# Kernel optimization log

Hardware: AMD Instinct MI355X
Metric: run time of the kernel (lower is better)

## Reference

```python
import jax, jax.numpy as jnp
import numpy as np

HIDDEN = 100


def gcn_conv(x, W, b, src, dst, w, n):
    # GCNConv with symmetric normalization (self-loops already appended).
    xw = x @ W                                   # [N, H]
    deg = jax.ops.segment_sum(w, dst, num_segments=n)
    dinv = jnp.where(deg > 0, jax.lax.rsqrt(deg), 0.0)
    norm = dinv[src] * w * dinv[dst]             # [E]
    agg = jax.ops.segment_sum(norm[:, None] * xw[src], dst, num_segments=n)
    return agg + b


def setup_inputs() -> dict:
    key = jax.random.key(0)
    ks = jax.random.split(key, 16)
    N, F, E, H = 100000, 128, 1600000, HIDDEN
    x = jax.random.normal(ks[0], (N, F), dtype=jnp.float32)
    edge_index = jax.random.randint(ks[1], (2, E), 0, N, dtype=jnp.int64)
    edge_weight = jax.random.uniform(ks[2], (E,), dtype=jnp.float32)
    sF = 1.0 / np.sqrt(F)
    sH2 = 1.0 / np.sqrt(2 * H)
    sH = 1.0 / np.sqrt(H)
    inp = {
        "x": x, "edge_index": edge_index, "edge_weight": edge_weight,
        "Wcz": jax.random.normal(ks[3], (F, H), jnp.float32) * sF,
        "bcz": jnp.zeros((H,), jnp.float32),
        "Wcr": jax.random.normal(ks[4], (F, H), jnp.float32) * sF,
        "bcr": jnp.zeros((H,), jnp.float32),
        "Wch": jax.random.normal(ks[5], (F, H), jnp.float32) * sF,
        "bch": jnp.zeros((H,), jnp.float32),
        "Wlz": jax.random.normal(ks[6], (2 * H, H), jnp.float32) * sH2,
        "blz": jnp.zeros((H,), jnp.float32),
        "Wlr": jax.random.normal(ks[7], (2 * H, H), jnp.float32) * sH2,
        "blr": jnp.zeros((H,), jnp.float32),
        "Wlh": jax.random.normal(ks[8], (2 * H, H), jnp.float32) * sH2,
        "blh": jnp.zeros((H,), jnp.float32),
        "Wout": jax.random.normal(ks[9], (H, 1), jnp.float32) * sH,
        "bout": jnp.zeros((1,), jnp.float32),
    }
    return inp


def reference(x, edge_index, edge_weight,
              Wcz, bcz, Wcr, bcr, Wch, bch,
              Wlz, blz, Wlr, blr, Wlh, blh,
              Wout, bout):
    N = x.shape[0]
    # add self-loops with weight 1 (GCNConv default)
    loop = jnp.arange(N, dtype=edge_index.dtype)
    src = jnp.concatenate([edge_index[0], loop])
    dst = jnp.concatenate([edge_index[1], loop])
    w = jnp.concatenate([edge_weight, jnp.ones((N,), edge_weight.dtype)])

    H0 = jnp.zeros((N, HIDDEN), x.dtype)  # TGCN initial hidden state

    cz = gcn_conv(x, Wcz, bcz, src, dst, w, N)
    Z = jax.nn.sigmoid(jnp.concatenate([cz, H0], axis=1) @ Wlz + blz)

    cr = gcn_conv(x, Wcr, bcr, src, dst, w, N)
    R = jax.nn.sigmoid(jnp.concatenate([cr, H0], axis=1) @ Wlr + blr)

    ch = gcn_conv(x, Wch, bch, src, dst, w, N)
    Ht = jnp.tanh(jnp.concatenate([ch, H0 * R], axis=1) @ Wlh + blh)

    Hn = Z * H0 + (1.0 - Z) * Ht
    h = jax.nn.relu(Hn)
    return h @ Wout + bout
```

## Files before the change

### kernel.cpp

```cpp
#include <hip/hip_runtime.h>

#define FEAT 128
#define HID  100
#define CHUNK 4096

typedef __attribute__((ext_vector_type(8))) short short8;
typedef __attribute__((ext_vector_type(4))) float f32x4;

__device__ __forceinline__ unsigned short f2bf(float f) {
    union { float f; unsigned int u; } v; v.f = f;
    unsigned int r = v.u + 0x7fffu + ((v.u >> 16) & 1u);
    return (unsigned short)(r >> 16);
}

__device__ __forceinline__ int get_edge(const void* ei, int f64, long long pos) {
    return f64 ? (int)((const long long*)ei)[pos] : ((const int*)ei)[pos];
}

__device__ __forceinline__ int detect_f64(const void* ei) {
    const int* p = (const int*)ei;
    unsigned long long b = __ballot(p[2 * (threadIdx.x & 63) + 1] == 0);
    return b == ~0ull;
}

__global__ __launch_bounds__(256)
void k_cvtfold(const float* __restrict__ x, uint4* __restrict__ xb, int n8,
               const float* __restrict__ Wcz, const float* __restrict__ bcz,
               const float* __restrict__ Wch, const float* __restrict__ bch,
               const float* __restrict__ Wlz, const float* __restrict__ blz,
               const float* __restrict__ Wlh, const float* __restrict__ blh,
               const float* __restrict__ Wout,
               unsigned short* __restrict__ WB, float* __restrict__ bfold_ext,
               float* __restrict__ WoutZ) {
    const int CVTB = 1024;
    if (blockIdx.x < CVTB) {
        int stride = CVTB * 256;
        for (int i = blockIdx.x * 256 + threadIdx.x; i < n8; i += stride) {
            float4 a = *(const float4*)(x + (size_t)i * 8);
            float4 b = *(const float4*)(x + (size_t)i * 8 + 4);
            uint4 o;
            o.x = f2bf(a.x) | ((unsigned)f2bf(a.y) << 16);
            o.y = f2bf(a.z) | ((unsigned)f2bf(a.w) << 16);
            o.z = f2bf(b.x) | ((unsigned)f2bf(b.y) << 16);
            o.w = f2bf(b.z) | ((unsigned)f2bf(b.w) << 16);
            xb[i] = o;
        }
        return;
    }
    int idx = (blockIdx.x - CVTB) * 256 + threadIdx.x;
    if (idx < FEAT * 256) {
        int k = idx >> 8, n = idx & 255;
        float val = 0.f;
        if (n < HID) {
            for (int m = 0; m < HID; m++) val += Wcz[k * HID + m] * Wlz[m * HID + n];
        } else if (n >= 128 && n < 128 + HID) {
            int c = n - 128;
            for (int m = 0; m < HID; m++) val += Wch[k * HID + m] * Wlh[m * HID + c];
        }
        int ni = n >> 4, lc = n & 15, ks = k >> 5, hi = (k >> 3) & 3, j = k & 7;
        WB[(((ni * 4 + ks) * 64 + hi * 16 + lc) << 3) + j] = f2bf(val);
    } else if (idx < FEAT * 256 + 256) {
        int c = idx - FEAT * 256;
        float v = 0.f;
        if (c < HID) {
            v = blz[c];
            for (int j = 0; j < HID; j++) v += bcz[j] * Wlz[j * HID + c];
        } else if (c >= 128 && c < 128 + HID) {
            int cc = c - 128;
            v = blh[cc];
            for (int j = 0; j < HID; j++) v += bch[j] * Wlh[j * HID + cc];
        }
        bfold_ext[c] = v;
    } else if (idx < FEAT * 256 + 256 + 128) {
        int c = idx - FEAT * 256 - 256;
        WoutZ[c] = (c < HID) ? Wout[c] : 0.f;
    }
}

__global__ __launch_bounds__(256)
void k_hist(const void* ei, int* __restrict__ bucketCnt, int* __restrict__ blockBase,
            int NB, int E) {
    int f64 = detect_f64(ei);
    __shared__ int hist[1024];
    int t = threadIdx.x;
    for (int i = t; i < NB; i += 256) hist[i] = 0;
    __syncthreads();
    int e0 = blockIdx.x * CHUNK;
#pragma unroll
    for (int k = 0; k < CHUNK / 256; k++) {
        int e = e0 + k * 256 + t;
        if (e < E) {
            int d = get_edge(ei, f64, (long long)E + e);
            atomicAdd(&hist[d >> 8], 1);
        }
    }
    __syncthreads();
    int* bb = blockBase + (size_t)blockIdx.x * NB;
    for (int b = t; b < NB; b += 256) {
        int c = hist[b];
        if (c) bb[b] = atomicAdd(&bucketCnt[b], c);
    }
}

__global__ void k_scanb(const int* __restrict__ bucketCnt, int* __restrict__ bucketStart,
                        int NB) {
    __shared__ int lds[1024];
    int t = threadIdx.x;
    int v = (t < NB) ? bucketCnt[t] : 0;
    lds[t] = v;
    __syncthreads();
    for (int off = 1; off < 1024; off <<= 1) {
        int tv = (t >= off) ? lds[t - off] : 0;
        __syncthreads();
        lds[t] += tv;
        __syncthreads();
    }
    if (t < NB) bucketStart[t] = lds[t] - v;
    if (t == NB - 1) bucketStart[NB] = lds[t];
}

__global__ __launch_bounds__(256)
void k_scatter(const void* ei, const float* __restrict__ w,
               const int* __restrict__ bucketStart, const int* __restrict__ blockBase,
               int2* __restrict__ sc, int NB, int E) {
    int f64 = detect_f64(ei);
    __shared__ int hist[1024];
    int t = threadIdx.x;
    for (int i = t; i < NB; i += 256) hist[i] = 0;
    __syncthreads();
    int e0 = blockIdx.x * CHUNK;
    const int* bb = blockBase + (size_t)blockIdx.x * NB;
#pragma unroll
    for (int k = 0; k < CHUNK / 256; k++) {
        int e = e0 + k * 256 + t;
        if (e < E) {
            int s = get_edge(ei, f64, e);
            int d = get_edge(ei, f64, (long long)E + e);
            int b = d >> 8;
            int r = atomicAdd(&hist[b], 1);
            int pos = bucketStart[b] + bb[b] + r;
            long long val = ((long long)__float_as_int(w[e]) << 32)
                          | (unsigned)(s | ((d & 255) << 24));
            __builtin_nontemporal_store(val, (long long*)&sc[pos]);
        }
    }
}

__global__ __launch_bounds__(256)
void k_bucket(const int2* __restrict__ sc, const int* __restrict__ bucketStart,
              int* __restrict__ offs, int* __restrict__ cnt,
              int2* __restrict__ csr, int N) {
    __shared__ int hist[256];
    __shared__ int offsL[256];
    __shared__ int rank[256];
    int t = threadIdx.x;
    int n0 = blockIdx.x << 8;
    int s = bucketStart[blockIdx.x], e = bucketStart[blockIdx.x + 1];
    hist[t] = 0;
    rank[t] = 0;
    __syncthreads();
    for (int i = s + t; i < e; i += 256)
        atomicAdd(&hist[((unsigned)sc[i].x) >> 24], 1);
    __syncthreads();
    int v = (n0 + t < N) ? hist[t] + 1 : 0;
    offsL[t] = v;
    __syncthreads();
    for (int off = 1; off < 256; off <<= 1) {
        int tv = (t >= off) ? offsL[t - off] : 0;
        __syncthreads();
        offsL[t] += tv;
        __syncthreads();
    }
    int myOff = offsL[t] - v;
    int csrBase = s + n0;
    if (n0 + t < N) {
        offs[n0 + t] = csrBase + myOff;
        cnt[n0 + t] = v;
    }
    offsL[t] = myOff;
    __syncthreads();
    for (int i = s + t; i < e; i += 256) {
        int2 en = sc[i];
        int dlow = ((unsigned)en.x) >> 24;
        int r = atomicAdd(&rank[dlow], 1);
        csr[csrBase + offsL[dlow] + r] = make_int2(en.x & 0xFFFFFF, en.y);
    }
}

__global__ __launch_bounds__(256)
void k_degsum(int2* __restrict__ csr, const int* __restrict__ offs,
              const int* __restrict__ cnt, float* __restrict__ dinv, int N) {
    int t = threadIdx.x;
    int sub = t & 15;
    long long node = (long long)blockIdx.x * 16 + (t >> 4);
    if (node >= N) return;
    int rs = offs[node], c = cnt[node];
    float s = 0.f;
    for (int i = sub; i < c - 1; i += 16) s += __int_as_float(csr[rs + i].y);
    s += __shfl_xor(s, 1);
    s += __shfl_xor(s, 2);
    s += __shfl_xor(s, 4);
    s += __shfl_xor(s, 8);
    if (sub == 0) {
        dinv[node] = rsqrtf(1.f + s);
        csr[rs + c - 1] = make_int2((int)node, __float_as_int(1.0f));
    }
}

__global__ __launch_bounds__(256)
void k_agg4(const unsigned short* __restrict__ xb, const float* __restrict__ dinv,
            const int* __restrict__ offs, const int* __restrict__ cnt,
            const int2* __restrict__ csr, unsigned short* __restrict__ aggx, int N) {
    int wid  = __builtin_amdgcn_readfirstlane(threadIdx.x >> 6);
    int lane = threadIdx.x & 63;
    long long node = (long long)blockIdx.x * 4 + wid;
    if (node >= N) return;
    int q  = lane >> 3;
    int fl = lane & 7;
    float acc[16];
#pragma unroll
    for (int j = 0; j < 16; j++) acc[j] = 0.f;
    int rs = offs[node];
    int c  = cnt[node];
    for (int i = q; i < c; i += 8) {
        int2 e = csr[rs + i];
        float nr = __int_as_float(e.y) * dinv[e.x];
        const uint4* xp = (const uint4*)(xb + (size_t)e.x * FEAT + fl * 16);
        uint4 v0 = xp[0];
        uint4 v1 = xp[1];
        const unsigned* u0 = &v0.x;
        const unsigned* u1 = &v1.x;
#pragma unroll
        for (int j = 0; j < 4; j++) {
            acc[2*j]         += nr * __uint_as_float(u0[j] << 16);
            acc[2*j + 1]     += nr * __uint_as_float(u0[j] & 0xffff0000u);
            acc[8 + 2*j]     += nr * __uint_as_float(u1[j] << 16);
            acc[8 + 2*j + 1] += nr * __uint_as_float(u1[j] & 0xffff0000u);
        }
    }
#pragma unroll
    for (int j = 0; j < 16; j++) {
        acc[j] += __shfl_xor(acc[j], 8);
        acc[j] += __shfl_xor(acc[j], 16);
        acc[j] += __shfl_xor(acc[j], 32);
    }
    if (q == 0) {
        float dn = dinv[node];
        uint4 o0, o1;
        unsigned* p0 = &o0.x;
        unsigned* p1 = &o1.x;
#pragma unroll
        for (int j = 0; j < 4; j++) {
            p0[j] = f2bf(acc[2*j] * dn)   | ((unsigned)f2bf(acc[2*j+1] * dn) << 16);
            p1[j] = f2bf(acc[8+2*j] * dn) | ((unsigned)f2bf(acc[8+2*j+1] * dn) << 16);
        }
        uint4* op = (uint4*)(aggx + (size_t)node * FEAT + fl * 16);
        op[0] = o0;
        op[1] = o1;
    }
}

__global__ __launch_bounds__(256)
void k_post3(const unsigned short* __restrict__ aggx, const unsigned short* __restrict__ WB,
             const float* __restrict__ bfold_ext, const float* __restrict__ WoutZ,
             const float* __restrict__ bout, float* __restrict__ out, int N) {
    __shared__ unsigned short At[64 * 136];
    __shared__ float red[64 * 4];
    int t = threadIdx.x;
    int lane = t & 63;
    int w = __builtin_amdgcn_readfirstlane(t >> 6);
    long long base = (long long)blockIdx.x * 64;

    for (int it = 0; it < 4; it++) {
        int idx = it * 256 + t;
        int row = idx >> 4, c16 = idx & 15;
        long long grow = base + row;
        uint4 v = make_uint4(0u, 0u, 0u, 0u);
        if (grow < N) v = *(const uint4*)(aggx + grow * FEAT + c16 * 8);
        *(uint4*)(At + row * 136 + c16 * 8) = v;
    }
    __syncthreads();

    int l15 = lane & 15, lhi = lane >> 4;
    int tadd = 2 * w;
    f32x4 acc[4][4];
#pragma unroll
    for (int ti = 0; ti < 4; ti++)
#pragma unroll
        for (int mi = 0; mi < 4; mi++) acc[ti][mi] = (f32x4)0.f;

    const int tiles[4] = {tadd, tadd + 1, tadd + 8, tadd + 9};
#pragma unroll
    for (int ks = 0; ks < 4; ks++) {
        short8 a[4];
#pragma unroll
        for (int mi = 0; mi < 4; mi++)
            a[mi] = *(const short8*)(At + (mi * 16 + l15) * 136 + ks * 32 + lhi * 8);
        short8 b[4];
#pragma unroll
        for (int ti = 0; ti < 4; ti++)
            b[ti] = *(const short8*)(WB + (((tiles[ti] * 4 + ks) * 64 + lane) << 3));
#pragma unroll
        for (int ti = 0; ti < 4; ti++)
#pragma unroll
            for (int mi = 0; mi < 4; mi++)
                acc[ti][mi] = __builtin_amdgcn_mfma_f32_16x16x32_bf16(
                    a[mi], b[ti], acc[ti][mi], 0, 0, 0);
    }

    float partial[4][4];
#pragma unroll
    for (int mi = 0; mi < 4; mi++)
#pragma unroll
        for (int r = 0; r < 4; r++) partial[mi][r] = 0.f;
#pragma unroll
    for (int d = 0; d < 2; d++) {
        int zcol = (tadd + d) * 16 + l15;
        float bz = bfold_ext[zcol];
        float bh = bfold_ext[zcol + 128];
        float wo = WoutZ[zcol];
#pragma unroll
        for (int mi = 0; mi < 4; mi++)
#pragma unroll
            for (int r = 0; r < 4; r++) {
                float az = acc[d][mi][r] + bz;
                float ah = acc[d + 2][mi][r] + bh;
                float z  = 1.f / (1.f + expf(-az));
                float ht = tanhf(ah);
                float h  = (1.f - z) * ht;
                h = h > 0.f ? h : 0.f;
                partial[mi][r] += h * wo;
            }
    }
#pragma unroll
    for (int mi = 0; mi < 4; mi++)
#pragma unroll
        for (int r = 0; r < 4; r++) {
            float p = partial[mi][r];
            p += __shfl_xor(p, 1);
            p += __shfl_xor(p, 2);
            p += __shfl_xor(p, 4);
            p += __shfl_xor(p, 8);
            partial[mi][r] = p;
        }
    if (l15 == 0) {
#pragma unroll
        for (int mi = 0; mi < 4; mi++)
#pragma unroll
            for (int r = 0; r < 4; r++)
                red[(mi * 16 + lhi * 4 + r) * 4 + w] = partial[mi][r];
    }
    __syncthreads();
    if (t < 64) {
        long long node = base + t;
        if (node < N)
            out[node] = red[t * 4] + red[t * 4 + 1] + red[t * 4 + 2] + red[t * 4 + 3]
                      + bout[0];
    }
}

extern "C" void kernel_launch(void* const* d_in, const int* in_sizes, int n_in,
                              void* d_out, int out_size, void* d_ws, size_t ws_size,
                              hipStream_t stream) {
    const float* x    = (const float*)d_in[0];
    const void*  ei   = d_in[1];
    const float* ew   = (const float*)d_in[2];
    const float* Wcz  = (const float*)d_in[3];
    const float* bcz  = (const float*)d_in[4];
    const float* Wch  = (const float*)d_in[7];
    const float* bch  = (const float*)d_in[8];
    const float* Wlz  = (const float*)d_in[9];
    const float* blz  = (const float*)d_in[10];
    const float* Wlh  = (const float*)d_in[13];
    const float* blh  = (const float*)d_in[14];
    const float* Wout = (const float*)d_in[15];
    const float* bout = (const float*)d_in[16];
    float* out = (float*)d_out;

    int N = in_sizes[0] / FEAT;
    int E = in_sizes[2];
    int NB = (N + 255) >> 8;
    int nblocksA = (E + CHUNK - 1) / CHUNK;

    char* p = (char*)d_ws;
    auto alloc = [&](size_t bytes) -> char* {
        char* r = p;
        p += (bytes + 255) & ~(size_t)255;
        return r;
    };
    float*          dinv        = (float*)alloc((size_t)N * 4);
    int*            cnt         = (int*)  alloc((size_t)N * 4);
    int*            offs        = (int*)  alloc((size_t)N * 4);
    int*            bucketCnt   = (int*)  alloc((size_t)(NB + 1) * 4);
    int*            bucketStart = (int*)  alloc((size_t)(NB + 1) * 4);
    int2*           csr         = (int2*) alloc((size_t)(E + N) * 8);
    unsigned short* xb          = (unsigned short*)alloc((size_t)N * FEAT * 2);
    unsigned short* aggx        = (unsigned short*)alloc((size_t)N * FEAT * 2);
    unsigned short* WB          = (unsigned short*)alloc((size_t)FEAT * 256 * 2);
    float*          bfold_ext   = (float*)alloc(256 * 4);
    float*          WoutZ       = (float*)alloc(128 * 4);
    int2* sc        = (int2*)aggx;
    int*  blockBase = (int*)((char*)aggx + (size_t)E * 8);

    hipMemsetAsync(bucketCnt, 0, (size_t)NB * 4, stream);
    k_cvtfold<<<1024 + (FEAT * 256 + 256 + 128 + 255) / 256, 256, 0, stream>>>(
        x, (uint4*)xb, N * FEAT / 8,
        Wcz, bcz, Wch, bch, Wlz, blz, Wlh, blh, Wout, WB, bfold_ext, WoutZ);
    k_hist<<<nblocksA, 256, 0, stream>>>(ei, bucketCnt, blockBase, NB, E);
    k_scanb<<<1, 1024, 0, stream>>>(bucketCnt, bucketStart, NB);
    k_scatter<<<nblocksA, 256, 0, stream>>>(ei, ew, bucketStart, blockBase, sc, NB, E);
    k_bucket<<<NB, 256, 0, stream>>>(sc, bucketStart, offs, cnt, csr, N);
    k_degsum<<<(N + 15) / 16, 256, 0, stream>>>(csr, offs, cnt, dinv, N);
    k_agg4<<<(N + 3) / 4, 256, 0, stream>>>(xb, dinv, offs, cnt, csr, aggx, N);
    k_post3<<<(N + 63) / 64, 256, 0, stream>>>(aggx, WB, bfold_ext, WoutZ, bout, out, N);
}
```

Measured before the change: 319.2 us.

## Fuse histogram into front kernel and degree sum into bucket sort

The edge histogram pass moves into the conversion/weight-fold kernel as an extra range of blocks, removing one launch and letting it overlap with the bf16 conversion. Weighted degree and the self-loop CSR entry are now computed inside k_bucket using LDS float atomics, which removes the separate k_degsum pass over the CSR. The aggregation kernel is also split into two launches over a hardcoded node boundary. The LDS float atomics make the degree summation order nondeterministic, and the split adds a launch.

```diff
diff --git a/kernel.cpp b/kernel.cpp
--- a/kernel.cpp
+++ b/kernel.cpp
@@ -24,15 +24,18 @@
 }
 
 __global__ __launch_bounds__(256)
-void k_cvtfold(const float* __restrict__ x, uint4* __restrict__ xb, int n8,
-               const float* __restrict__ Wcz, const float* __restrict__ bcz,
-               const float* __restrict__ Wch, const float* __restrict__ bch,
-               const float* __restrict__ Wlz, const float* __restrict__ blz,
-               const float* __restrict__ Wlh, const float* __restrict__ blh,
-               const float* __restrict__ Wout,
-               unsigned short* __restrict__ WB, float* __restrict__ bfold_ext,
-               float* __restrict__ WoutZ) {
-    const int CVTB = 1024;
+void k_front(const float* __restrict__ x, uint4* __restrict__ xb, int n8,
+             const float* __restrict__ Wcz, const float* __restrict__ bcz,
+             const float* __restrict__ Wch, const float* __restrict__ bch,
+             const float* __restrict__ Wlz, const float* __restrict__ blz,
+             const float* __restrict__ Wlh, const float* __restrict__ blh,
+             const float* __restrict__ Wout,
+             unsigned short* __restrict__ WB, float* __restrict__ bfold_ext,
+             float* __restrict__ WoutZ,
+             const void* ei, int* __restrict__ bucketCnt,
+             int* __restrict__ blockBase, int NB, int E) {
+    const int CVTB = 1024, FOLDB = 130;
+    __shared__ int hist[1024];
     if (blockIdx.x < CVTB) {
         int stride = CVTB * 256;
         for (int i = blockIdx.x * 256 + threadIdx.x; i < n8; i += stride) {
@@ -47,45 +50,43 @@
         }
         return;
     }
-    int idx = (blockIdx.x - CVTB) * 256 + threadIdx.x;
-    if (idx < FEAT * 256) {
-        int k = idx >> 8, n = idx & 255;
-        float val = 0.f;
-        if (n < HID) {
-            for (int m = 0; m < HID; m++) val += Wcz[k * HID + m] * Wlz[m * HID + n];
-        } else if (n >= 128 && n < 128 + HID) {
-            int c = n - 128;
-            for (int m = 0; m < HID; m++) val += Wch[k * HID + m] * Wlh[m * HID + c];
-        }
-        int ni = n >> 4, lc = n & 15, ks = k >> 5, hi = (k >> 3) & 3, j = k & 7;
-        WB[(((ni * 4 + ks) * 64 + hi * 16 + lc) << 3) + j] = f2bf(val);
-    } else if (idx < FEAT * 256 + 256) {
-        int c = idx - FEAT * 256;
-        float v = 0.f;
-        if (c < HID) {
-            v = blz[c];
-            for (int j = 0; j < HID; j++) v += bcz[j] * Wlz[j * HID + c];
-        } else if (c >= 128 && c < 128 + HID) {
-            int cc = c - 128;
-            v = blh[cc];
-            for (int j = 0; j < HID; j++) v += bch[j] * Wlh[j * HID + cc];
-        }
-        bfold_ext[c] = v;
-    } else if (idx < FEAT * 256 + 256 + 128) {
-        int c = idx - FEAT * 256 - 256;
-        WoutZ[c] = (c < HID) ? Wout[c] : 0.f;
-    }
-}
-
-__global__ __launch_bounds__(256)
-void k_hist(const void* ei, int* __restrict__ bucketCnt, int* __restrict__ blockBase,
-            int NB, int E) {
+    if (blockIdx.x < CVTB + FOLDB) {
+        int idx = (blockIdx.x - CVTB) * 256 + threadIdx.x;
+        if (idx < FEAT * 256) {
+            int k = idx >> 8, n = idx & 255;
+            float val = 0.f;
+            if (n < HID) {
+                for (int m = 0; m < HID; m++) val += Wcz[k * HID + m] * Wlz[m * HID + n];
+            } else if (n >= 128 && n < 128 + HID) {
+                int c = n - 128;
+                for (int m = 0; m < HID; m++) val += Wch[k * HID + m] * Wlh[m * HID + c];
+            }
+            int ni = n >> 4, lc = n & 15, ks = k >> 5, hi = (k >> 3) & 3, j = k & 7;
+            WB[(((ni * 4 + ks) * 64 + hi * 16 + lc) << 3) + j] = f2bf(val);
+        } else if (idx < FEAT * 256 + 256) {
+            int c = idx - FEAT * 256;
+            float v = 0.f;
+            if (c < HID) {
+                v = blz[c];
+                for (int j = 0; j < HID; j++) v += bcz[j] * Wlz[j * HID + c];
+            } else if (c >= 128 && c < 128 + HID) {
+                int cc = c - 128;
+                v = blh[cc];
+                for (int j = 0; j < HID; j++) v += bch[j] * Wlh[j * HID + cc];
+            }
+            bfold_ext[c] = v;
+        } else if (idx < FEAT * 256 + 256 + 128) {
+            int c = idx - FEAT * 256 - 256;
+            WoutZ[c] = (c < HID) ? Wout[c] : 0.f;
+        }
+        return;
+    }
     int f64 = detect_f64(ei);
-    __shared__ int hist[1024];
+    int cb = blockIdx.x - CVTB - FOLDB;
     int t = threadIdx.x;
     for (int i = t; i < NB; i += 256) hist[i] = 0;
     __syncthreads();
-    int e0 = blockIdx.x * CHUNK;
+    int e0 = cb * CHUNK;
 #pragma unroll
     for (int k = 0; k < CHUNK / 256; k++) {
         int e = e0 + k * 256 + t;
@@ -95,7 +96,7 @@
         }
     }
     __syncthreads();
-    int* bb = blockBase + (size_t)blockIdx.x * NB;
+    int* bb = blockBase + (size_t)cb * NB;
     for (int b = t; b < NB; b += 256) {
         int c = hist[b];
         if (c) bb[b] = atomicAdd(&bucketCnt[b], c);
@@ -149,15 +150,17 @@
 __global__ __launch_bounds__(256)
 void k_bucket(const int2* __restrict__ sc, const int* __restrict__ bucketStart,
               int* __restrict__ offs, int* __restrict__ cnt,
-              int2* __restrict__ csr, int N) {
+              int2* __restrict__ csr, float* __restrict__ dinv, int N) {
     __shared__ int hist[256];
     __shared__ int offsL[256];
     __shared__ int rank[256];
+    __shared__ float wsum[256];
     int t = threadIdx.x;
     int n0 = blockIdx.x << 8;
     int s = bucketStart[blockIdx.x], e = bucketStart[blockIdx.x + 1];
     hist[t] = 0;
     rank[t] = 0;
+    wsum[t] = 0.f;
     __syncthreads();
     for (int i = s + t; i < e; i += 256)
         atomicAdd(&hist[((unsigned)sc[i].x) >> 24], 1);
@@ -184,37 +187,24 @@
         int dlow = ((unsigned)en.x) >> 24;
         int r = atomicAdd(&rank[dlow], 1);
         csr[csrBase + offsL[dlow] + r] = make_int2(en.x & 0xFFFFFF, en.y);
-    }
-}
-
-__global__ __launch_bounds__(256)
-void k_degsum(int2* __restrict__ csr, const int* __restrict__ offs,
-              const int* __restrict__ cnt, float* __restrict__ dinv, int N) {
-    int t = threadIdx.x;
-    int sub = t & 15;
-    long long node = (long long)blockIdx.x * 16 + (t >> 4);
-    if (node >= N) return;
-    int rs = offs[node], c = cnt[node];
-    float s = 0.f;
-    for (int i = sub; i < c - 1; i += 16) s += __int_as_float(csr[rs + i].y);
-    s += __shfl_xor(s, 1);
-    s += __shfl_xor(s, 2);
-    s += __shfl_xor(s, 4);
-    s += __shfl_xor(s, 8);
-    if (sub == 0) {
-        dinv[node] = rsqrtf(1.f + s);
-        csr[rs + c - 1] = make_int2((int)node, __float_as_int(1.0f));
+        atomicAdd(&wsum[dlow], __int_as_float(en.y));
+    }
+    __syncthreads();
+    if (n0 + t < N) {
+        dinv[n0 + t] = rsqrtf(1.f + wsum[t]);
+        csr[csrBase + myOff + hist[t]] = make_int2(n0 + t, __float_as_int(1.0f));
     }
 }
 
 __global__ __launch_bounds__(256)
 void k_agg4(const unsigned short* __restrict__ xb, const float* __restrict__ dinv,
             const int* __restrict__ offs, const int* __restrict__ cnt,
-            const int2* __restrict__ csr, unsigned short* __restrict__ aggx, int N) {
+            const int2* __restrict__ csr, unsigned short* __restrict__ aggx,
+            int nlo, int nhi) {
     int wid  = __builtin_amdgcn_readfirstlane(threadIdx.x >> 6);
     int lane = threadIdx.x & 63;
-    long long node = (long long)blockIdx.x * 4 + wid;
-    if (node >= N) return;
+    long long node = (long long)nlo + blockIdx.x * 4 + wid;
+    if (node >= nhi) return;
     int q  = lane >> 3;
     int fl = lane & 7;
     float acc[16];
@@ -403,14 +393,15 @@
     int*  blockBase = (int*)((char*)aggx + (size_t)E * 8);
 
     hipMemsetAsync(bucketCnt, 0, (size_t)NB * 4, stream);
-    k_cvtfold<<<1024 + (FEAT * 256 + 256 + 128 + 255) / 256, 256, 0, stream>>>(
+    k_front<<<1024 + 130 + nblocksA, 256, 0, stream>>>(
         x, (uint4*)xb, N * FEAT / 8,
-        Wcz, bcz, Wch, bch, Wlz, blz, Wlh, blh, Wout, WB, bfold_ext, WoutZ);
-    k_hist<<<nblocksA, 256, 0, stream>>>(ei, bucketCnt, blockBase, NB, E);
+        Wcz, bcz, Wch, bch, Wlz, blz, Wlh, blh, Wout, WB, bfold_ext, WoutZ,
+        ei, bucketCnt, blockBase, NB, E);
     k_scanb<<<1, 1024, 0, stream>>>(bucketCnt, bucketStart, NB);
     k_scatter<<<nblocksA, 256, 0, stream>>>(ei, ew, bucketStart, blockBase, sc, NB, E);
-    k_bucket<<<NB, 256, 0, stream>>>(sc, bucketStart, offs, cnt, csr, N);
-    k_degsum<<<(N + 15) / 16, 256, 0, stream>>>(csr, offs, cnt, dinv, N);
-    k_agg4<<<(N + 3) / 4, 256, 0, stream>>>(xb, dinv, offs, cnt, csr, aggx, N);
+    k_bucket<<<NB, 256, 0, stream>>>(sc, bucketStart, offs, cnt, csr, dinv, N);
+    int N2 = 50000;
+    k_agg4<<<(N2 + 3) / 4, 256, 0, stream>>>(xb, dinv, offs, cnt, csr, aggx, 0, N2);
+    k_agg4<<<(N - N2 + 3) / 4, 256, 0, stream>>>(xb, dinv, offs, cnt, csr, aggx, N2, N);
     k_post3<<<(N + 63) / 64, 256, 0, stream>>>(aggx, WB, bfold_ext, WoutZ, bout, out, N);
 }
```

Result: no change. 319.4 us (+0.1%).
